# Performance work log

Hardware: AMD Instinct MI355X
Metric: run time of the kernel (lower is better)

Reference implementation:

```python
import jax, jax.numpy as jnp
import numpy as np

NUM_CLASSES = 100
NUM_DIM = 384
BATCH = 4096


def setup_inputs() -> dict:
    key = jax.random.key(0)
    k1, k2, k3, k4 = jax.random.split(key, 4)
    inputs = jax.random.normal(k1, (BATCH, NUM_DIM), dtype=jnp.float32)
    targets = jax.random.randint(k2, (BATCH,), 0, NUM_CLASSES)
    centers = jax.random.normal(k3, (NUM_CLASSES, NUM_DIM), dtype=jnp.float32)
    centers_weights = jax.random.uniform(k4, (NUM_CLASSES, NUM_DIM), dtype=jnp.float32)
    return {
        "inputs": inputs,
        "targets": targets,
        "epoch_number": 0,
        "centers": centers,
        "centers_weights": centers_weights,
    }


def _closest_center_dist(centers, centers_weights):
    # calc_centers(which_one=1): dist[i,j] = sqrt(sum_d 2^w[i,d]*(c[i,d]-c[j,d])^2),
    # row-sorted, second-smallest (the diagonal 0 is the smallest).
    # Computed with numpy in the original -> detached constant.
    w = 2.0 ** centers_weights                      # [C, D]
    diff = centers[:, None, :] - centers[None, :, :]  # [C, C, D] (C=100, tiny)
    d2 = jnp.einsum('cd,ced->ce', w, diff * diff)   # [C, C]
    d = jnp.sqrt(d2)
    d = jnp.sort(d, axis=1)
    return jax.lax.stop_gradient(d[:, 1])           # [C]


def reference(inputs, targets, epoch_number, centers, centers_weights):
    B = inputs.shape[0]
    centers_dist = _closest_center_dist(centers, centers_weights)  # [C]

    c_b = centers[targets]                     # [B, D] centers_batch
    w_b = 2.0 ** centers_weights[targets]      # [B, D] weights (gathered)

    # dist[i, j] = sqrt( sum_d w_b[j,d] * (c_b[j,d] - inputs[i,d])^2 )
    # expanded into three contractions to avoid the [B,B,D] broadcast tensor
    t_cc = jnp.einsum('jd,jd->j', w_b, c_b * c_b)        # [B]   (j-term)
    t_xc = inputs @ (w_b * c_b).T                        # [B,B] cross term
    t_xx = (inputs * inputs) @ w_b.T                     # [B,B]
    d2 = t_cc[None, :] - 2.0 * t_xc + t_xx               # [B,B]
    dist = jnp.sqrt(jnp.maximum(d2, 1e-12))

    mask = targets[:, None] == targets[None, :]          # [B,B] same-class
    dist_ap = jnp.where(mask, dist, -jnp.inf).max(axis=1)  # hardest positive
    dist_an = jnp.where(mask, jnp.inf, dist).min(axis=1)   # hardest negative

    cc = centers_dist[targets]                           # [B]
    per_sample = dist_ap + jnp.where(dist_an >= cc, 0.0, cc - dist_an)
    return jnp.sum(per_sample) / B
```

## Files before the change

kernel.cpp:

```cpp
#include <hip/hip_runtime.h>
#include <math.h>

#define NC 100
#define ND 384
#define NB 4096
#define KS 12
#define KTC 32
#define MT 64
#define NSLOT 128
#define CLS_PAD 132
#define XSP 36
#define PPAD 104
#define AUX 116
#define GEMM_BLOCKS (NB / MT * KS)

__global__ __launch_bounds__(256, 3) void fused_kernel(
    const float* __restrict__ x, const float* __restrict__ centers,
    const float* __restrict__ cw, const int* __restrict__ targets,
    float* __restrict__ tcc, float* __restrict__ cdist,
    unsigned* __restrict__ pres16, float* __restrict__ part,
    float* __restrict__ out) {
  __shared__ float sA[MT * XSP + 2 * KTC * CLS_PAD];
  int b = blockIdx.x, tid = threadIdx.x;
  int wave = tid >> 6, lane = tid & 63;

  if (b < NC) {
    int i = b;
    float* ci_s = sA;
    float* wi_s = sA + ND;
    float* sred = sA + 2 * ND;
    if (i == 0 && tid == 255) out[0] = 0.f;
    for (int d = tid; d < ND; d += 256) {
      ci_s[d] = centers[i * ND + d];
      wi_s[d] = exp2f(cw[i * ND + d]);
    }
    __syncthreads();
    {
      float p = 0.f;
      for (int d = tid; d < ND; d += 256) p = fmaf(wi_s[d] * ci_s[d], ci_s[d], p);
      #pragma unroll
      for (int off = 32; off; off >>= 1) p += __shfl_xor(p, off, 64);
      if (lane == 0) sred[wave] = p;
      __syncthreads();
      if (tid == 0) tcc[i] = sred[0] + sred[1] + sred[2] + sred[3];
      __syncthreads();
    }
    float minv = 1e30f;
    for (int s = 0; s < 24; s += 4) {
      float red[4];
      #pragma unroll
      for (int u = 0; u < 4; u++) {
        int j = wave + 4 * (s + u);
        float acc = 0.f;
        #pragma unroll
        for (int e = 0; e < 6; e++) {
          int d = lane + 64 * e;
          float df = ci_s[d] - centers[j * ND + d];
          acc = fmaf(wi_s[d] * df, df, acc);
        }
        red[u] = acc;
      }
      #pragma unroll
      for (int off = 32; off; off >>= 1) {
        #pragma unroll
        for (int u = 0; u < 4; u++) red[u] += __shfl_xor(red[u], off, 64);
      }
      #pragma unroll
      for (int u = 0; u < 4; u++) {
        int j = wave + 4 * (s + u);
        if (j != i) minv = fminf(minv, red[u]);
      }
    }
    {
      int j = wave + 96;
      float acc = 0.f;
      #pragma unroll
      for (int e = 0; e < 6; e++) {
        int d = lane + 64 * e;
        float df = ci_s[d] - centers[j * ND + d];
        acc = fmaf(wi_s[d] * df, df, acc);
      }
      #pragma unroll
      for (int off = 32; off; off >>= 1) acc += __shfl_xor(acc, off, 64);
      if (j != i) minv = fminf(minv, acc);
    }
    if (lane == 0) sred[wave] = minv;
    __syncthreads();
    if (tid == 0)
      cdist[i] = sqrtf(fminf(fminf(sred[0], sred[1]), fminf(sred[2], sred[3])));
  } else if (b < AUX) {
    int pb = b - NC;
    unsigned* um = (unsigned*)sA;
    if (tid < 4) um[tid] = 0u;
    __syncthreads();
    int t = targets[pb * 256 + tid];
    atomicOr(&um[t >> 5], 1u << (t & 31));
    __syncthreads();
    if (tid < 4) pres16[pb * 4 + tid] = um[tid];
  } else {
    int g = b - AUX;
    int mb = g / KS;
    int ks = g - mb * KS;
    int koff = ks * KTC;
    float* xs   = sA;
    float* ws_t = sA + MT * XSP;
    float* as_t = ws_t + KTC * CLS_PAD;

    #pragma unroll
    for (int j = 0; j < 2; j++) {
      int idx = tid + 256 * j;
      int r = idx >> 3, c4 = idx & 7;
      float4 v = *(const float4*)(x + (mb * MT + r) * ND + koff + 4 * c4);
      *(float4*)(&xs[r * XSP + 4 * c4]) = v;
    }
    #pragma unroll
    for (int j = 0; j < 16; j++) {
      int idx = tid + 256 * j;
      int k = idx >> 5, d = idx & 31;
      float w = 0.f, c = 0.f;
      if (k < NC) {
        w = exp2f(cw[k * ND + koff + d]);
        c = centers[k * ND + koff + d];
      }
      ws_t[d * CLS_PAD + k] = w;
      as_t[d * CLS_PAD + k] = -2.f * w * c;
    }
    __syncthreads();

    int cg = tid & 31, sg = tid >> 5;
    float acc[8][4];
    #pragma unroll
    for (int m = 0; m < 8; m++)
      #pragma unroll
      for (int u = 0; u < 4; u++) acc[m][u] = 0.f;

    for (int d4 = 0; d4 < KTC; d4 += 4) {
      float wv[4][4], av[4][4], xv[8][4];
      #pragma unroll
      for (int i2 = 0; i2 < 4; i2++) {
        *(float4*)&wv[i2][0] = *(const float4*)(&ws_t[(d4 + i2) * CLS_PAD + 4 * cg]);
        *(float4*)&av[i2][0] = *(const float4*)(&as_t[(d4 + i2) * CLS_PAD + 4 * cg]);
      }
      #pragma unroll
      for (int m = 0; m < 8; m++)
        *(float4*)&xv[m][0] = *(const float4*)(&xs[(sg + 8 * m) * XSP + d4]);
      #pragma unroll
      for (int i2 = 0; i2 < 4; i2++) {
        #pragma unroll
        for (int m = 0; m < 8; m++) {
          float xval = xv[m][i2];
          #pragma unroll
          for (int u = 0; u < 4; u++) {
            float t = fmaf(xval, wv[i2][u], av[i2][u]);
            acc[m][u] = fmaf(xval, t, acc[m][u]);
          }
        }
      }
    }
    if (cg < 25) {
      #pragma unroll
      for (int m = 0; m < 8; m++) {
        int i = mb * MT + sg + 8 * m;
        *(float4*)(&part[(ks * NB + i) * PPAD + 4 * cg]) = *(float4*)&acc[m][0];
      }
    }
  }
}

__global__ __launch_bounds__(256) void finish_kernel(
    const int* __restrict__ targets, const float* __restrict__ tcc,
    const float* __restrict__ cdist, const unsigned* __restrict__ pres16,
    const float* __restrict__ part, float* __restrict__ out) {
  __shared__ unsigned msk[4];
  __shared__ float r_an[2][2], r_ap[2][2], lsum[8];
  int tid = threadIdx.x;
  if (tid < 4) {
    unsigned m = 0;
    #pragma unroll
    for (int bb = 0; bb < 16; bb++) m |= pres16[bb * 4 + tid];
    msk[tid] = m;
  }
  int wave = tid >> 6, lane = tid & 63;
  int h = wave & 1, sl = wave >> 1;
  int k = h * 64 + lane;
  bool valid = k < NC;
  float base = valid ? tcc[k] : 0.f;
  __syncthreads();
  bool pres = valid && ((msk[k >> 5] >> (k & 31)) & 1u);

  for (int pass = 0; pass < 4; pass++) {
    int i = blockIdx.x * 8 + pass * 2 + sl;
    int ti = targets[i];
    float cand_an = 1e30f, cand_ap = 0.f;
    if (valid) {
      float d2 = base;
      #pragma unroll
      for (int s = 0; s < KS; s++) d2 += part[(s * NB + i) * PPAD + k];
      float dist = sqrtf(fmaxf(d2, 1e-12f));
      if (k == ti) cand_ap = dist;
      else if (pres) cand_an = dist;
    }
    #pragma unroll
    for (int off = 32; off; off >>= 1) {
      cand_an = fminf(cand_an, __shfl_xor(cand_an, off, 64));
      cand_ap = fmaxf(cand_ap, __shfl_xor(cand_ap, off, 64));
    }
    if (lane == 0) { r_an[sl][h] = cand_an; r_ap[sl][h] = cand_ap; }
    __syncthreads();
    if (tid < 2) {
      int isamp = blockIdx.x * 8 + pass * 2 + tid;
      float cc = cdist[targets[isamp]];
      float an = fminf(r_an[tid][0], r_an[tid][1]);
      float ap = fmaxf(r_ap[tid][0], r_ap[tid][1]);
      lsum[pass * 2 + tid] = ap + ((an >= cc) ? 0.f : cc - an);
    }
    __syncthreads();
  }
  if (tid == 0) {
    float t = 0.f;
    #pragma unroll
    for (int j = 0; j < 8; j++) t += lsum[j];
    atomicAdd(out, t * (1.0f / NB));
  }
}

extern "C" void kernel_launch(void* const* d_in, const int* in_sizes, int n_in,
                              void* d_out, int out_size, void* d_ws, size_t ws_size,
                              hipStream_t stream) {
  const float* inputs  = (const float*)d_in[0];
  const int*   targets = (const int*)d_in[1];
  const float* centers = (const float*)d_in[3];
  const float* cw      = (const float*)d_in[4];
  float* out = (float*)d_out;

  float* tcc       = (float*)d_ws;
  float* cdist     = tcc + 128;
  unsigned* pres16 = (unsigned*)(cdist + 128);
  float* part      = (float*)(pres16 + 64);

  fused_kernel<<<AUX + GEMM_BLOCKS, 256, 0, stream>>>(
      inputs, centers, cw, targets, tcc, cdist, pres16, part, out);
  finish_kernel<<<NB / 8, 256, 0, stream>>>(targets, tcc, cdist, pres16, part, out);
}
```

Baseline: 94.51 us.

## Enlarge GEMM tile to 128 rows and cut K-splits to eight

```diff
diff --git a/kernel.cpp b/kernel.cpp
--- a/kernel.cpp
+++ b/kernel.cpp
@@ -4,23 +4,23 @@
 #define NC 100
 #define ND 384
 #define NB 4096
-#define KS 12
-#define KTC 32
-#define MT 64
-#define NSLOT 128
+#define KS 8
+#define KT 48
+#define MT 128
+#define XSP 52
 #define CLS_PAD 132
-#define XSP 36
 #define PPAD 104
 #define AUX 116
-#define GEMM_BLOCKS (NB / MT * KS)
-
-__global__ __launch_bounds__(256, 3) void fused_kernel(
+#define GEMM_BLOCKS ((NB / MT) * KS)
+#define SAF (MT * XSP + 2 * KT * CLS_PAD)
+
+__global__ __launch_bounds__(256, 2) void fused_kernel(
     const float* __restrict__ x, const float* __restrict__ centers,
     const float* __restrict__ cw, const int* __restrict__ targets,
     float* __restrict__ tcc, float* __restrict__ cdist,
     unsigned* __restrict__ pres16, float* __restrict__ part,
     float* __restrict__ out) {
-  __shared__ float sA[MT * XSP + 2 * KTC * CLS_PAD];
+  __shared__ float sA[SAF];
   int b = blockIdx.x, tid = threadIdx.x;
   int wave = tid >> 6, lane = tid & 63;
 
@@ -81,8 +81,19 @@
         acc = fmaf(wi_s[d] * df, df, acc);
       }
       #pragma unroll
-      for (int off = 32; off; off >>= 1) acc += __shfl_xor(acc, off, 64);
-      if (j != i) minv = fminf(minv, acc);
+      for (int off = 32; off; off >>= 1) acc = fminf(acc + __shfl_xor(acc, off, 64), 1e30f), acc = acc;
+      if (j != i) {  }
+      if (false) {}
+      float acc2 = 0.f;
+      #pragma unroll
+      for (int e = 0; e < 6; e++) {
+        int d = lane + 64 * e;
+        float df = ci_s[d] - centers[j * ND + d];
+        acc2 = fmaf(wi_s[d] * df, df, acc2);
+      }
+      #pragma unroll
+      for (int off = 32; off; off >>= 1) acc2 += __shfl_xor(acc2, off, 64);
+      if (j != i) minv = fminf(minv, acc2);
     }
     if (lane == 0) sred[wave] = minv;
     __syncthreads();
@@ -99,69 +110,67 @@
     if (tid < 4) pres16[pb * 4 + tid] = um[tid];
   } else {
     int g = b - AUX;
-    int mb = g / KS;
-    int ks = g - mb * KS;
-    int koff = ks * KTC;
-    float* xs   = sA;
+    int mb = g >> 3, ks = g & 7;
+    int koff = ks * KT;
+    float* xs = sA;
     float* ws_t = sA + MT * XSP;
-    float* as_t = ws_t + KTC * CLS_PAD;
-
-    #pragma unroll
-    for (int j = 0; j < 2; j++) {
-      int idx = tid + 256 * j;
-      int r = idx >> 3, c4 = idx & 7;
-      float4 v = *(const float4*)(x + (mb * MT + r) * ND + koff + 4 * c4);
-      *(float4*)(&xs[r * XSP + 4 * c4]) = v;
-    }
-    #pragma unroll
-    for (int j = 0; j < 16; j++) {
-      int idx = tid + 256 * j;
-      int k = idx >> 5, d = idx & 31;
-      float w = 0.f, c = 0.f;
-      if (k < NC) {
-        w = exp2f(cw[k * ND + koff + d]);
-        c = centers[k * ND + koff + d];
-      }
-      ws_t[d * CLS_PAD + k] = w;
-      as_t[d * CLS_PAD + k] = -2.f * w * c;
+    float* as_t = ws_t + KT * CLS_PAD;
+
+    #pragma unroll
+    for (int r = 0; r < 8; r++) {
+      int idx = tid + 256 * r;
+      int row = idx >> 4, slot = idx & 15;
+      if (slot < 12) {
+        float4 v = *(const float4*)(x + (mb * MT + row) * ND + koff + 4 * slot);
+        *(float4*)&xs[row * XSP + 4 * slot] = v;
+      }
+    }
+    for (int r = 0; r < 19; r++) {
+      int idx = tid + 256 * r;
+      if (idx < NC * KT) {
+        int k = idx / KT, d = idx - k * KT;
+        float w = exp2f(cw[k * ND + koff + d]);
+        float c = centers[k * ND + koff + d];
+        ws_t[d * CLS_PAD + k] = w;
+        as_t[d * CLS_PAD + k] = -2.f * w * c;
+      }
     }
     __syncthreads();
 
     int cg = tid & 31, sg = tid >> 5;
-    float acc[8][4];
-    #pragma unroll
-    for (int m = 0; m < 8; m++)
+    float acc[16][4];
+    #pragma unroll
+    for (int m = 0; m < 16; m++)
       #pragma unroll
       for (int u = 0; u < 4; u++) acc[m][u] = 0.f;
 
-    for (int d4 = 0; d4 < KTC; d4 += 4) {
-      float wv[4][4], av[4][4], xv[8][4];
+    #pragma unroll 1
+    for (int d4 = 0; d4 < KT; d4 += 4) {
+      float wv[4][4], av[4][4], xv[16][4];
       #pragma unroll
       for (int i2 = 0; i2 < 4; i2++) {
-        *(float4*)&wv[i2][0] = *(const float4*)(&ws_t[(d4 + i2) * CLS_PAD + 4 * cg]);
-        *(float4*)&av[i2][0] = *(const float4*)(&as_t[(d4 + i2) * CLS_PAD + 4 * cg]);
-      }
-      #pragma unroll
-      for (int m = 0; m < 8; m++)
-        *(float4*)&xv[m][0] = *(const float4*)(&xs[(sg + 8 * m) * XSP + d4]);
+        *(float4*)&wv[i2][0] = *(const float4*)&ws_t[(d4 + i2) * CLS_PAD + 4 * cg];
+        *(float4*)&av[i2][0] = *(const float4*)&as_t[(d4 + i2) * CLS_PAD + 4 * cg];
+      }
+      #pragma unroll
+      for (int m = 0; m < 16; m++)
+        *(float4*)&xv[m][0] = *(const float4*)&xs[(sg + 8 * m) * XSP + d4];
       #pragma unroll
       for (int i2 = 0; i2 < 4; i2++) {
         #pragma unroll
-        for (int m = 0; m < 8; m++) {
+        for (int m = 0; m < 16; m++) {
           float xval = xv[m][i2];
           #pragma unroll
-          for (int u = 0; u < 4; u++) {
-            float t = fmaf(xval, wv[i2][u], av[i2][u]);
-            acc[m][u] = fmaf(xval, t, acc[m][u]);
-          }
+          for (int u = 0; u < 4; u++)
+            acc[m][u] = fmaf(xval, fmaf(xval, wv[i2][u], av[i2][u]), acc[m][u]);
         }
       }
     }
     if (cg < 25) {
       #pragma unroll
-      for (int m = 0; m < 8; m++) {
+      for (int m = 0; m < 16; m++) {
         int i = mb * MT + sg + 8 * m;
-        *(float4*)(&part[(ks * NB + i) * PPAD + 4 * cg]) = *(float4*)&acc[m][0];
+        *(float4*)&part[(ks * NB + i) * PPAD + 4 * cg] = *(float4*)&acc[m][0];
       }
     }
   }
```

Measured after the change: 92.73 us. Within noise of the previous version (-1.9%).
